# Performance work log

Measured on AMD Instinct MI355X. Metric: run time of the kernel, lower is better.

Reference implementation:

```python
import jax, jax.numpy as jnp
import numpy as np

B, C, H, W = 2, 64, 128, 128   # batch, z_dim, square feature map (original code requires H == W)
Q = 8192                       # query points per image
HID = 128                      # hidden_node
DIMS = [C * 9 + 4, HID, HID, HID, HID, C]
EPS_SHIFT = 1e-6
EPS_CLAMP = 1e-6


def setup_inputs():
    key = jax.random.key(0)
    ks = jax.random.split(key, 13)
    x = jax.random.normal(ks[0], (B, C, H, W), jnp.float32)
    coord = jax.random.uniform(ks[1], (B, Q, 2), jnp.float32, minval=-1.0, maxval=1.0)
    cell = jnp.full((B, Q, 2), 2.0 / 256.0, jnp.float32)  # cell of a 256x256 target grid
    inp = {"x": x, "coord": coord, "cell": cell}
    for i in range(5):
        fin, fout = DIMS[i], DIMS[i + 1]
        bound = 1.0 / np.sqrt(fin)
        inp[f"w{i}"] = jax.random.uniform(ks[3 + 2 * i], (fin, fout), jnp.float32, minval=-bound, maxval=bound)
        inp[f"b{i}"] = jax.random.uniform(ks[4 + 2 * i], (fout,), jnp.float32, minval=-bound, maxval=bound)
    return inp


def _unfold3x3(x):
    # F.unfold(x, 3, padding=1).view(B, C*9, H, W); channel order c*9 + (ky*3 + kx)
    b, c, h, w = x.shape
    xp = jnp.pad(x, ((0, 0), (0, 0), (1, 1), (1, 1)))
    pats = jnp.stack([xp[:, :, ky:ky + h, kx:kx + w] for ky in range(3) for kx in range(3)], axis=2)
    return pats.reshape(b, c * 9, h, w)


def _nearest_idx(g, n):
    # grid_sample mode='nearest', align_corners=False
    ix = ((g + 1.0) * n - 1.0) / 2.0
    return jnp.clip(jnp.round(ix), 0, n - 1).astype(jnp.int32)


def _liif_forward(x, coord, cell, w0, b0, w1, b1, w2, b2, w3, b3, w4, b4):
    b, c, h, w = x.shape
    feat = _unfold3x3(x)                                     # [B, 9C, H, W]
    feat_flat = feat.transpose(0, 2, 3, 1).reshape(b, h * w, 9 * c)
    # make_coord pixel-center sequence; H == W so one seq serves both axes
    seq = -1.0 + 1.0 / h + (2.0 / h) * jnp.arange(h, dtype=jnp.float32)
    rx = 1.0 / h   # 2 / H / 2
    ry = 1.0 / w
    hid_ws = [w0, w1, w2, w3]
    hid_bs = [b0, b1, b2, b3]
    scale = jnp.array([h, w], dtype=coord.dtype)
    rel_cell = cell * scale
    preds, areas = [], []
    for vx in (-1, 1):
        for vy in (-1, 1):
            c0 = jnp.clip(coord[..., 0] + vx * rx + EPS_SHIFT, -1 + EPS_CLAMP, 1 - EPS_CLAMP)
            c1 = jnp.clip(coord[..., 1] + vy * ry + EPS_SHIFT, -1 + EPS_CLAMP, 1 - EPS_CLAMP)
            # coord_.flip(-1): grid x (width) = coord[...,1], grid y (height) = coord[...,0]
            iy = _nearest_idx(c0, h)
            ix = _nearest_idx(c1, w)
            lin = iy * w + ix                                            # [B, Q]
            q_feat = jnp.take_along_axis(feat_flat, lin[..., None], axis=1)  # [B, Q, 9C]
            # feat_coord built with meshgrid(indexing='xy'): channel0 = seq[ix], channel1 = seq[iy]
            rel0 = (coord[..., 0] - seq[ix]) * h
            rel1 = (coord[..., 1] - seq[iy]) * w
            inp = jnp.concatenate([q_feat, rel0[..., None], rel1[..., None], rel_cell], axis=-1)
            hdd = inp
            for wi, bi in zip(hid_ws, hid_bs):
                hdd = jax.nn.relu(hdd @ wi + bi)
            preds.append(hdd @ w4 + b4)                                  # [B, Q, C]
            areas.append(jnp.abs(rel0 * rel1) + 1e-9)
    tot = areas[0] + areas[1] + areas[2] + areas[3]
    perm = (3, 2, 1, 0)   # original swaps areas 0<->3 and 1<->2
    ret = preds[0] * (areas[perm[0]] / tot)[..., None]
    for i in range(1, 4):
        ret = ret + preds[i] * (areas[perm[i]] / tot)[..., None]
    return ret


def reference(x, coord, cell, w0, b0, w1, b1, w2, b2, w3, b3, w4, b4):
    return _liif_forward(x, coord, cell, w0, b0, w1, b1, w2, b2, w3, b3, w4, b4)
```

## Files before the change

### kernel.cpp

```cpp
#include <hip/hip_runtime.h>


typedef unsigned short U16;
typedef unsigned int   u32;
using f16x8  = __attribute__((ext_vector_type(8)))  _Float16;
using f32x4  = __attribute__((ext_vector_type(4)))  float;
using f32x16 = __attribute__((ext_vector_type(16))) float;
using u16x8  = __attribute__((ext_vector_type(8)))  U16;
using u16x4  = __attribute__((ext_vector_type(4)))  U16;

#define P_OFF    2097152
#define W0F_OFF  6291456
#define W1F_OFF  6365184
#define W4F_OFF  6414336

__device__ __forceinline__ float h2f(U16 u){ _Float16 h; __builtin_memcpy(&h,&u,2); return (float)h; }
__device__ __forceinline__ U16 f2h(float f){ _Float16 h = (_Float16)f; U16 u; __builtin_memcpy(&u,&h,2); return u; }
__device__ __forceinline__ u32 packf16(float a, float b){
  _Float16 ha = (_Float16)a, hb = (_Float16)b;
  U16 ua, ub; __builtin_memcpy(&ua,&ha,2); __builtin_memcpy(&ub,&hb,2);
  return (u32)ua | ((u32)ub << 16);
}
__device__ __forceinline__ f16x8 bfrag(const u32* w){
  union { u32 u[4]; f16x8 v; } t;
  t.u[0]=w[0]; t.u[1]=w[1]; t.u[2]=w[2]; t.u[3]=w[3];
  return t.v;
}

__device__ __forceinline__ int nearest_idx(float g){
  float t = (g + 1.0f) * 128.0f;
  t = (t - 1.0f) * 0.5f;
  float r = rintf(t);
  r = fminf(fmaxf(r, 0.0f), 127.0f);
  return (int)r;
}
__device__ __forceinline__ float seqv(int i){ return -0.9921875f + 0.015625f*(float)i; }

__device__ __forceinline__ void corner_calc(float c0, float c1, int corner,
                                            int& iy, int& ix, float& rel0, float& rel1){
  const float rx = 0.0078125f;
  float sx = (corner & 2) ? rx : -rx;
  float sy = (corner & 1) ? rx : -rx;
  float a0 = c0 + sx; a0 = a0 + 1e-6f; a0 = fminf(fmaxf(a0, -1.0f + 1e-6f), 1.0f - 1e-6f);
  float a1 = c1 + sy; a1 = a1 + 1e-6f; a1 = fminf(fmaxf(a1, -1.0f + 1e-6f), 1.0f - 1e-6f);
  iy = nearest_idx(a0);
  ix = nearest_idx(a1);
  rel0 = (c0 - seqv(ix)) * 128.0f;
  rel1 = (c1 - seqv(iy)) * 128.0f;
}

__global__ __launch_bounds__(256) void k_prepw(
    const float* __restrict__ w0, const float* __restrict__ w1,
    const float* __restrict__ w2, const float* __restrict__ w3,
    const float* __restrict__ w4, U16* __restrict__ ws)
{
  __shared__ U16 sh[64 * 72];
  const int tid = threadIdx.x, bid = blockIdx.x;

  if (bid < 24) {
    int L = bid >> 3, s = bid & 7;
    const float* src = (L == 0) ? w1 : (L == 1) ? w2 : w3;
    {
      int kk = tid >> 4, m0 = (tid & 15) << 3;
      const float* p = src + (((s << 4) + kk) << 7) + m0;
      float4 a = *(const float4*)p, b2v = *(const float4*)(p + 4);
      U16* d = &sh[kk * 128 + m0];
      d[0]=f2h(a.x); d[1]=f2h(a.y); d[2]=f2h(a.z); d[3]=f2h(a.w);
      d[4]=f2h(b2v.x); d[5]=f2h(b2v.y); d[6]=f2h(b2v.z); d[7]=f2h(b2v.w);
    }
    __syncthreads();
    {
      int mt = tid >> 6, lane = tid & 63;
      u16x8 o;
      #pragma unroll
      for (int e = 0; e < 8; ++e)
        o[e] = sh[((((lane >> 5) << 3) + e) << 7) + (mt << 5) + (lane & 31)];
      *(u16x8*)(ws + W1F_OFF + (L << 14) + (((s << 2) + mt) << 9) + (lane << 3)) = o;
    }
  } else if (bid < 32) {
    int s = bid - 24;
    {
      int kk = tid >> 4, m0 = (tid & 15) << 2;
      float4 a = *(const float4*)(w4 + (((s << 4) + kk) << 6) + m0);
      U16* d = &sh[kk * 64 + m0];
      d[0]=f2h(a.x); d[1]=f2h(a.y); d[2]=f2h(a.z); d[3]=f2h(a.w);
    }
    __syncthreads();
    if (tid < 128) {
      int mt4 = tid >> 6, lane = tid & 63;
      u16x8 o;
      #pragma unroll
      for (int e = 0; e < 8; ++e)
        o[e] = sh[((((lane >> 5) << 3) + e) << 6) + (mt4 << 5) + (lane & 31)];
      *(u16x8*)(ws + W4F_OFF + (((s << 1) + mt4) << 9) + (lane << 3)) = o;
    }
  } else {
    int t2 = bid - 32, kpos = t2 >> 1, ks = t2 & 1;
    {
      int cc = tid >> 3, o0 = (tid & 7) << 4;
      const float* p = w0 + ((size_t)((((ks << 5) + cc) * 9) + kpos) << 7) + o0;
      #pragma unroll
      for (int j = 0; j < 4; ++j) {
        float4 v = *(const float4*)(p + (j << 2));
        U16* d = &sh[(cc << 7) + o0 + (j << 2)];
        d[0]=f2h(v.x); d[1]=f2h(v.y); d[2]=f2h(v.z); d[3]=f2h(v.w);
      }
    }
    __syncthreads();
    {
      int lane = tid & 63, mt0 = tid >> 6;
      #pragma unroll
      for (int i = 0; i < 2; ++i) {
        int mtile = mt0 + (i << 2);
        u16x8 o;
        #pragma unroll
        for (int e = 0; e < 8; ++e)
          o[e] = sh[((((lane >> 4) << 3) + e) << 7) + (mtile << 4) + (lane & 15)];
        *(u16x8*)(ws + W0F_OFF + (((((kpos << 1) + ks) << 3) + mtile) << 9) + (lane << 3)) = o;
      }
    }
  }
}

__global__ __launch_bounds__(256) void k_stage1(const float* __restrict__ x,
                                                const U16* __restrict__ w0f,
                                                const float* __restrict__ b0,
                                                U16* __restrict__ P)
{
  __shared__ U16 araw[3 * 66 * 64];
  const int tid = threadIdx.x, bid = blockIdx.x;
  const int b = bid >> 8, rem = bid & 255;
  const int y = rem >> 1, x0 = (rem & 1) << 6;

  {
    int c = tid & 63, dy = tid >> 6;
    if (dy < 3) {
      int yy = y + dy - 1;
      bool rowok = (yy >= 0) && (yy < 128);
      const float* xr = rowok
        ? (x + ((((size_t)b << 6) + c) << 14) + ((size_t)yy << 7)) : x;
      U16* arow = &araw[(dy * 66) * 64];
      {
        float v0 = 0.0f, v65 = 0.0f;
        if (rowok && x0 > 0)        v0  = xr[x0 - 1];
        if (rowok && x0 + 64 < 128) v65 = xr[x0 + 64];
        arow[0 * 64 + c] = f2h(v0);
        arow[65 * 64 + (c ^ 8)] = f2h(v65);
      }
      if (rowok) {
        #pragma unroll
        for (int g = 0; g < 16; ++g) {
          float4 v = *(const float4*)(xr + x0 + (g << 2));
          #pragma unroll
          for (int j = 0; j < 4; ++j) {
            int xp = 1 + (g << 2) + j;
            float vj = (j == 0) ? v.x : (j == 1) ? v.y : (j == 2) ? v.z : v.w;
            arow[xp * 64 + (c ^ ((xp & 7) << 3))] = f2h(vj);
          }
        }
      } else {
        #pragma unroll
        for (int xp = 1; xp <= 64; ++xp)
          arow[xp * 64 + (c ^ ((xp & 7) << 3))] = f2h(0.0f);
      }
    }
  }
  __syncthreads();

  const int wv = tid >> 6, ln = tid & 63;
  const int lrow = ln & 15, lg = ln >> 4;

  f32x4 acc[2][4];
  #pragma unroll
  for (int m = 0; m < 2; ++m)
    #pragma unroll
    for (int n = 0; n < 4; ++n) acc[m][n] = (f32x4){0.f, 0.f, 0.f, 0.f};

  #pragma unroll
  for (int kpos = 0; kpos < 9; ++kpos) {
    const int dyr = kpos / 3;
    const int dx = kpos % 3 - 1;
    f16x8 a[2][2];
    #pragma unroll
    for (int mf = 0; mf < 2; ++mf)
      #pragma unroll
      for (int ks = 0; ks < 2; ++ks) {
        size_t off = ((size_t)((((kpos << 1) + ks) << 3) + ((wv << 1) + mf)) << 9) + (ln << 3);
        a[mf][ks] = *(const f16x8*)(w0f + off);
      }
    #pragma unroll
    for (int ks = 0; ks < 2; ++ks)
      #pragma unroll
      for (int nf = 0; nf < 4; ++nf) {
        int xp = (nf << 4) + lrow + dx + 1;
        int cc = ((ks << 5) + (lg << 3)) ^ ((xp & 7) << 3);
        f16x8 bf = *(const f16x8*)(&araw[(dyr * 66 + xp) * 64 + cc]);
        acc[0][nf] = __builtin_amdgcn_mfma_f32_16x16x32_f16(a[0][ks], bf, acc[0][nf], 0, 0, 0);
        acc[1][nf] = __builtin_amdgcn_mfma_f32_16x16x32_f16(a[1][ks], bf, acc[1][nf], 0, 0, 0);
      }
  }

  #pragma unroll
  for (int mf = 0; mf < 2; ++mf) {
    int o0 = (wv << 5) + (mf << 4) + (lg << 2);
    float bb[4];
    #pragma unroll
    for (int r = 0; r < 4; ++r) bb[r] = b0[o0 + r];
    #pragma unroll
    for (int nf = 0; nf < 4; ++nf) {
      int px = x0 + (nf << 4) + lrow;
      u16x4 w;
      #pragma unroll
      for (int r = 0; r < 4; ++r) w[r] = f2h(acc[mf][nf][r] + bb[r]);
      *(u16x4*)(P + ((size_t)((b << 14) + (y << 7) + px)) * 128 + o0) = w;
    }
  }
}

__global__ __launch_bounds__(256) void k_stage2(
    const U16* __restrict__ P,
    const float* __restrict__ coord, const float* __restrict__ cell,
    const float* __restrict__ w0,
    const U16* __restrict__ w1f, const U16* __restrict__ w2f,
    const U16* __restrict__ w3f, const U16* __restrict__ w4f,
    const float* __restrict__ b1, const float* __restrict__ b2,
    const float* __restrict__ b3, const float* __restrict__ b4,
    float* __restrict__ out)
{
  const int tid = threadIdx.x;
  const int wv = tid >> 6, ln = tid & 63;
  const int wave = blockIdx.x * 4 + wv;
  const int q0 = wave << 3;
  const int col = ln & 31, h = ln >> 5;
  const int qi = col >> 2, c = col & 3;
  const int gq = q0 + qi;
  const int bimg = gq >> 13;

  float c0v = coord[gq * 2 + 0], c1v = coord[gq * 2 + 1];
  float rc0 = cell[gq * 2 + 0] * 128.0f, rc1 = cell[gq * 2 + 1] * 128.0f;
  int lin4[4]; float r0v[4], r1v[4], area[4];
  #pragma unroll
  for (int c4 = 0; c4 < 4; ++c4) {
    int iy, ix; float r0, r1;
    corner_calc(c0v, c1v, c4, iy, ix, r0, r1);
    lin4[c4] = iy * 128 + ix;
    r0v[c4] = r0; r1v[c4] = r1;
    area[c4] = fabsf(r0 * r1) + 1e-9f;
  }
  float tot = ((area[0] + area[1]) + area[2]) + area[3];
  float wgt = area[3 - c] / tot;
  float rel0 = r0v[c], rel1 = r1v[c];

  const U16* Pr = P + ((size_t)(bimg << 14) + lin4[c]) * 128;
  u16x8 pv[8];
  #pragma unroll
  for (int s = 0; s < 8; ++s)
    pv[s] = *(const u16x8*)(Pr + (s << 4) + (h << 3));

  u32 Bf[8][4];
  {
    const float* tu = w0 + 576 * 128;
    const float* tv = tu + 128;
    const float* ts2 = tv + 128;
    const float* tt = ts2 + 128;
    #pragma unroll
    for (int s = 0; s < 8; ++s) {
      int k0 = (s << 4) + (h << 3);
      f32x4 ua = *(const f32x4*)(tu + k0),  ub = *(const f32x4*)(tu + k0 + 4);
      f32x4 va = *(const f32x4*)(tv + k0),  vb = *(const f32x4*)(tv + k0 + 4);
      f32x4 sa = *(const f32x4*)(ts2 + k0), sb = *(const f32x4*)(ts2 + k0 + 4);
      f32x4 ta = *(const f32x4*)(tt + k0),  tb = *(const f32x4*)(tt + k0 + 4);
      float hh[8];
      #pragma unroll
      for (int e = 0; e < 8; ++e) {
        float uu = (e < 4) ? ua[e & 3] : ub[e & 3];
        float vvv = (e < 4) ? va[e & 3] : vb[e & 3];
        float ss = (e < 4) ? sa[e & 3] : sb[e & 3];
        float t2 = (e < 4) ? ta[e & 3] : tb[e & 3];
        hh[e] = fmaxf(h2f(pv[s][e]) + rel0 * uu + rel1 * vvv + rc0 * ss + rc1 * t2, 0.0f);
      }
      #pragma unroll
      for (int w = 0; w < 4; ++w)
        Bf[s][w] = packf16(hh[2 * w], hh[2 * w + 1]);
    }
  }

  const U16* wf_[3] = {w1f, w2f, w3f};
  const float* bL_[3] = {b1, b2, b3};
  #pragma unroll
  for (int L = 0; L < 3; ++L) {
    const U16* wf = wf_[L];
    const float* bL = bL_[L];
    f32x16 acc[4];
    #pragma unroll
    for (int mt = 0; mt < 4; ++mt)
      #pragma unroll
      for (int j = 0; j < 4; ++j) {
        f32x4 bv = *(const f32x4*)(bL + (mt << 5) + (j << 3) + (h << 2));
        #pragma unroll
        for (int q = 0; q < 4; ++q) acc[mt][4 * j + q] = bv[q];
      }
    #pragma unroll
    for (int s = 0; s < 8; ++s) {
      f16x8 B = bfrag(Bf[s]);
      #pragma unroll
      for (int mt = 0; mt < 4; ++mt) {
        f16x8 A = *(const f16x8*)(wf + (((size_t)(s * 4 + mt) * 64 + ln) << 3));
        acc[mt] = __builtin_amdgcn_mfma_f32_32x32x16_f16(A, B, acc[mt], 0, 0, 0);
      }
    }
    #pragma unroll
    for (int mtp = 0; mtp < 4; ++mtp) {
      u32 p[8];
      #pragma unroll
      for (int j2 = 0; j2 < 8; ++j2)
        p[j2] = packf16(fmaxf(acc[mtp][2 * j2], 0.0f), fmaxf(acc[mtp][2 * j2 + 1], 0.0f));
      #pragma unroll
      for (int u = 0; u < 2; ++u)
        #pragma unroll
        for (int w = 0; w < 2; ++w) {
          u32 va = p[w + 4 * u], vb = p[w + 4 * u + 2];
          asm("v_permlane32_swap_b32 %0, %1" : "+v"(va), "+v"(vb));
          Bf[2 * mtp + u][w]     = va;
          Bf[2 * mtp + u][w + 2] = vb;
        }
    }
  }

  f32x16 a4[2];
  #pragma unroll
  for (int mt4 = 0; mt4 < 2; ++mt4)
    #pragma unroll
    for (int r = 0; r < 16; ++r) a4[mt4][r] = 0.0f;
  #pragma unroll
  for (int s = 0; s < 8; ++s) {
    f16x8 B = bfrag(Bf[s]);
    #pragma unroll
    for (int mt4 = 0; mt4 < 2; ++mt4) {
      f16x8 A = *(const f16x8*)(w4f + (((size_t)(s * 2 + mt4) * 64 + ln) << 3));
      a4[mt4] = __builtin_amdgcn_mfma_f32_32x32x16_f16(A, B, a4[mt4], 0, 0, 0);
    }
  }

  float tacc[2][16];
  #pragma unroll
  for (int mt4 = 0; mt4 < 2; ++mt4)
    #pragma unroll
    for (int r = 0; r < 16; ++r) {
      float v = a4[mt4][r] * wgt;
      v += __shfl_xor(v, 1, 64);
      v += __shfl_xor(v, 2, 64);
      tacc[mt4][r] = v;
    }

  if (c == 0) {
    #pragma unroll
    for (int mt4 = 0; mt4 < 2; ++mt4)
      #pragma unroll
      for (int j = 0; j < 4; ++j) {
        int mo = (mt4 << 5) + (j << 3) + (h << 2);
        f32x4 bv = *(const f32x4*)(b4 + mo);
        f32x4 res;
        #pragma unroll
        for (int q = 0; q < 4; ++q) res[q] = tacc[mt4][4 * j + q] + bv[q];
        *(f32x4*)(out + (size_t)gq * 64 + mo) = res;
      }
  }
}

extern "C" void kernel_launch(void* const* d_in, const int* in_sizes, int n_in,
                              void* d_out, int out_size, void* d_ws, size_t ws_size,
                              hipStream_t stream)
{
  const float* x     = (const float*)d_in[0];
  const float* coord = (const float*)d_in[1];
  const float* cell  = (const float*)d_in[2];
  const float* w0    = (const float*)d_in[3];
  const float* b0    = (const float*)d_in[4];
  const float* w1    = (const float*)d_in[5];
  const float* b1    = (const float*)d_in[6];
  const float* w2    = (const float*)d_in[7];
  const float* b2    = (const float*)d_in[8];
  const float* w3    = (const float*)d_in[9];
  const float* b3    = (const float*)d_in[10];
  const float* w4    = (const float*)d_in[11];
  const float* b4    = (const float*)d_in[12];
  U16* ws = (U16*)d_ws;

  hipLaunchKernelGGL(k_prepw,  dim3(50),  dim3(256), 0, stream, w0, w1, w2, w3, w4, ws);
  hipLaunchKernelGGL(k_stage1, dim3(512), dim3(256), 0, stream,
                     x, ws + W0F_OFF, b0, ws + P_OFF);
  hipLaunchKernelGGL(k_stage2, dim3(512), dim3(256), 0, stream,
                     ws + P_OFF, coord, cell, w0,
                     ws + W1F_OFF, ws + W1F_OFF + 16384, ws + W1F_OFF + 32768, ws + W4F_OFF,
                     b1, b2, b3, b4, (float*)d_out);
}
```

Baseline: 44.44 us.

## Switch stage2 MLP to 16x16x32 MFMA with 4 queries per wave

Rewrites the per-query MLP in stage2 to use 16x16x32 f16 MFMA tiles instead of 32x32x16. Each wave now handles 4 queries (16 columns) rather than 8, and the grid doubles to 1024 blocks. The weight pre-swizzle in k_prepw is rewritten for the new fragment layout. The layer-to-layer fragment reshuffle now uses __shfl instead of permlane32 swaps. Smaller accumulators cut register pressure, and launch bounds request 4 blocks per SM to raise occupancy. The cost is more weight-fragment loads per query and extra cross-lane shuffle traffic.

```diff
diff --git a/kernel.cpp b/kernel.cpp
--- a/kernel.cpp
+++ b/kernel.cpp
@@ -5,14 +5,13 @@
 typedef unsigned int   u32;
 using f16x8  = __attribute__((ext_vector_type(8)))  _Float16;
 using f32x4  = __attribute__((ext_vector_type(4)))  float;
-using f32x16 = __attribute__((ext_vector_type(16))) float;
 using u16x8  = __attribute__((ext_vector_type(8)))  U16;
 using u16x4  = __attribute__((ext_vector_type(4)))  U16;
 
 #define P_OFF    2097152
 #define W0F_OFF  6291456
-#define W1F_OFF  6365184
-#define W4F_OFF  6414336
+#define W1G_OFF  6365184
+#define W4G_OFF  6414336
 
 __device__ __forceinline__ float h2f(U16 u){ _Float16 h; __builtin_memcpy(&h,&u,2); return (float)h; }
 __device__ __forceinline__ U16 f2h(float f){ _Float16 h = (_Float16)f; U16 u; __builtin_memcpy(&u,&h,2); return u; }
@@ -57,45 +56,53 @@
   __shared__ U16 sh[64 * 72];
   const int tid = threadIdx.x, bid = blockIdx.x;
 
-  if (bid < 24) {
-    int L = bid >> 3, s = bid & 7;
+  if (bid < 12) {
+    int L = bid >> 2, ks = bid & 3;
     const float* src = (L == 0) ? w1 : (L == 1) ? w2 : w3;
     {
-      int kk = tid >> 4, m0 = (tid & 15) << 3;
-      const float* p = src + (((s << 4) + kk) << 7) + m0;
-      float4 a = *(const float4*)p, b2v = *(const float4*)(p + 4);
-      U16* d = &sh[kk * 128 + m0];
+      int kl = tid >> 3, m0 = (tid & 7) << 4;
+      const float* p = src + (((ks << 5) + kl) << 7) + m0;
+      #pragma unroll
+      for (int j = 0; j < 4; ++j) {
+        float4 v = *(const float4*)(p + (j << 2));
+        U16* d = &sh[(kl << 7) + m0 + (j << 2)];
+        d[0]=f2h(v.x); d[1]=f2h(v.y); d[2]=f2h(v.z); d[3]=f2h(v.w);
+      }
+    }
+    __syncthreads();
+    {
+      int lane = tid & 63, mtb = tid >> 6;
+      #pragma unroll
+      for (int i = 0; i < 2; ++i) {
+        int mt = mtb + (i << 2);
+        u16x8 o;
+        #pragma unroll
+        for (int e = 0; e < 8; ++e)
+          o[e] = sh[((((lane >> 4) << 3) + e) << 7) + (mt << 4) + (lane & 15)];
+        *(u16x8*)(ws + W1G_OFF + (L << 14) + (((ks << 3) + mt) << 9) + (lane << 3)) = o;
+      }
+    }
+  } else if (bid < 16) {
+    int ks = bid - 12;
+    {
+      int kl = tid >> 3, m0 = (tid & 7) << 3;
+      const float* p = w4 + (((ks << 5) + kl) << 6) + m0;
+      float4 a = *(const float4*)p, b2 = *(const float4*)(p + 4);
+      U16* d = &sh[(kl << 6) + m0];
       d[0]=f2h(a.x); d[1]=f2h(a.y); d[2]=f2h(a.z); d[3]=f2h(a.w);
-      d[4]=f2h(b2v.x); d[5]=f2h(b2v.y); d[6]=f2h(b2v.z); d[7]=f2h(b2v.w);
+      d[4]=f2h(b2.x); d[5]=f2h(b2.y); d[6]=f2h(b2.z); d[7]=f2h(b2.w);
     }
     __syncthreads();
     {
-      int mt = tid >> 6, lane = tid & 63;
+      int lane = tid & 63, mt4 = tid >> 6;
       u16x8 o;
       #pragma unroll
       for (int e = 0; e < 8; ++e)
-        o[e] = sh[((((lane >> 5) << 3) + e) << 7) + (mt << 5) + (lane & 31)];
-      *(u16x8*)(ws + W1F_OFF + (L << 14) + (((s << 2) + mt) << 9) + (lane << 3)) = o;
-    }
-  } else if (bid < 32) {
-    int s = bid - 24;
-    {
-      int kk = tid >> 4, m0 = (tid & 15) << 2;
-      float4 a = *(const float4*)(w4 + (((s << 4) + kk) << 6) + m0);
-      U16* d = &sh[kk * 64 + m0];
-      d[0]=f2h(a.x); d[1]=f2h(a.y); d[2]=f2h(a.z); d[3]=f2h(a.w);
-    }
-    __syncthreads();
-    if (tid < 128) {
-      int mt4 = tid >> 6, lane = tid & 63;
-      u16x8 o;
-      #pragma unroll
-      for (int e = 0; e < 8; ++e)
-        o[e] = sh[((((lane >> 5) << 3) + e) << 6) + (mt4 << 5) + (lane & 31)];
-      *(u16x8*)(ws + W4F_OFF + (((s << 1) + mt4) << 9) + (lane << 3)) = o;
+        o[e] = sh[((((lane >> 4) << 3) + e) << 6) + (mt4 << 4) + (lane & 15)];
+      *(u16x8*)(ws + W4G_OFF + (((ks << 2) + mt4) << 9) + (lane << 3)) = o;
     }
   } else {
-    int t2 = bid - 32, kpos = t2 >> 1, ks = t2 & 1;
+    int t2 = bid - 16, kpos = t2 >> 1, ks = t2 & 1;
     {
       int cc = tid >> 3, o0 = (tid & 7) << 4;
       const float* p = w0 + ((size_t)((((ks << 5) + cc) * 9) + kpos) << 7) + o0;
@@ -217,12 +224,12 @@
   }
 }
 
-__global__ __launch_bounds__(256) void k_stage2(
+__global__ __launch_bounds__(256, 4) void k_stage2(
     const U16* __restrict__ P,
     const float* __restrict__ coord, const float* __restrict__ cell,
     const float* __restrict__ w0,
-    const U16* __restrict__ w1f, const U16* __restrict__ w2f,
-    const U16* __restrict__ w3f, const U16* __restrict__ w4f,
+    const U16* __restrict__ w1g, const U16* __restrict__ w2g,
+    const U16* __restrict__ w3g, const U16* __restrict__ w4g,
     const float* __restrict__ b1, const float* __restrict__ b2,
     const float* __restrict__ b3, const float* __restrict__ b4,
     float* __restrict__ out)
@@ -230,9 +237,9 @@
   const int tid = threadIdx.x;
   const int wv = tid >> 6, ln = tid & 63;
   const int wave = blockIdx.x * 4 + wv;
-  const int q0 = wave << 3;
-  const int col = ln & 31, h = ln >> 5;
-  const int qi = col >> 2, c = col & 3;
+  const int q0 = wave << 2;
+  const int c = ln & 15, h = ln >> 4;
+  const int qi = c >> 2, cc = c & 3;
   const int gq = q0 + qi;
   const int bimg = gq >> 13;
 
@@ -248,24 +255,20 @@
     area[c4] = fabsf(r0 * r1) + 1e-9f;
   }
   float tot = ((area[0] + area[1]) + area[2]) + area[3];
-  float wgt = area[3 - c] / tot;
-  float rel0 = r0v[c], rel1 = r1v[c];
-
-  const U16* Pr = P + ((size_t)(bimg << 14) + lin4[c]) * 128;
-  u16x8 pv[8];
-  #pragma unroll
-  for (int s = 0; s < 8; ++s)
-    pv[s] = *(const u16x8*)(Pr + (s << 4) + (h << 3));
-
-  u32 Bf[8][4];
+  float wgt = area[3 - cc] / tot;
+  float rel0 = r0v[cc], rel1 = r1v[cc];
+
+  u32 Bf[4][4];
   {
+    const U16* Pr = P + ((size_t)(bimg << 14) + lin4[cc]) * 128;
     const float* tu = w0 + 576 * 128;
     const float* tv = tu + 128;
     const float* ts2 = tv + 128;
     const float* tt = ts2 + 128;
     #pragma unroll
-    for (int s = 0; s < 8; ++s) {
-      int k0 = (s << 4) + (h << 3);
+    for (int ks = 0; ks < 4; ++ks) {
+      int k0 = (ks << 5) + (h << 3);
+      u16x8 pvv = *(const u16x8*)(Pr + k0);
       f32x4 ua = *(const f32x4*)(tu + k0),  ub = *(const f32x4*)(tu + k0 + 4);
       f32x4 va = *(const f32x4*)(tv + k0),  vb = *(const f32x4*)(tv + k0 + 4);
       f32x4 sa = *(const f32x4*)(ts2 + k0), sb = *(const f32x4*)(ts2 + k0 + 4);
@@ -273,98 +276,96 @@
       float hh[8];
       #pragma unroll
       for (int e = 0; e < 8; ++e) {
-        float uu = (e < 4) ? ua[e & 3] : ub[e & 3];
+        float uu  = (e < 4) ? ua[e & 3] : ub[e & 3];
         float vvv = (e < 4) ? va[e & 3] : vb[e & 3];
-        float ss = (e < 4) ? sa[e & 3] : sb[e & 3];
-        float t2 = (e < 4) ? ta[e & 3] : tb[e & 3];
-        hh[e] = fmaxf(h2f(pv[s][e]) + rel0 * uu + rel1 * vvv + rc0 * ss + rc1 * t2, 0.0f);
+        float ss  = (e < 4) ? sa[e & 3] : sb[e & 3];
+        float t2  = (e < 4) ? ta[e & 3] : tb[e & 3];
+        hh[e] = fmaxf(h2f(pvv[e]) + rel0 * uu + rel1 * vvv + rc0 * ss + rc1 * t2, 0.0f);
       }
       #pragma unroll
       for (int w = 0; w < 4; ++w)
-        Bf[s][w] = packf16(hh[2 * w], hh[2 * w + 1]);
-    }
-  }
-
-  const U16* wf_[3] = {w1f, w2f, w3f};
-  const float* bL_[3] = {b1, b2, b3};
+        Bf[ks][w] = packf16(hh[2 * w], hh[2 * w + 1]);
+    }
+  }
+
+  const int base = ((h & 1) << 5) | c;
+  const bool hi = (h & 2) != 0;
+
   #pragma unroll
   for (int L = 0; L < 3; ++L) {
-    const U16* wf = wf_[L];
-    const float* bL = bL_[L];
-    f32x16 acc[4];
-    #pragma unroll
-    for (int mt = 0; mt < 4; ++mt)
-      #pragma unroll
-      for (int j = 0; j < 4; ++j) {
-        f32x4 bv = *(const f32x4*)(bL + (mt << 5) + (j << 3) + (h << 2));
-        #pragma unroll
-        for (int q = 0; q < 4; ++q) acc[mt][4 * j + q] = bv[q];
-      }
-    #pragma unroll
-    for (int s = 0; s < 8; ++s) {
-      f16x8 B = bfrag(Bf[s]);
-      #pragma unroll
-      for (int mt = 0; mt < 4; ++mt) {
-        f16x8 A = *(const f16x8*)(wf + (((size_t)(s * 4 + mt) * 64 + ln) << 3));
-        acc[mt] = __builtin_amdgcn_mfma_f32_32x32x16_f16(A, B, acc[mt], 0, 0, 0);
-      }
-    }
-    #pragma unroll
-    for (int mtp = 0; mtp < 4; ++mtp) {
-      u32 p[8];
-      #pragma unroll
-      for (int j2 = 0; j2 < 8; ++j2)
-        p[j2] = packf16(fmaxf(acc[mtp][2 * j2], 0.0f), fmaxf(acc[mtp][2 * j2 + 1], 0.0f));
-      #pragma unroll
-      for (int u = 0; u < 2; ++u)
-        #pragma unroll
-        for (int w = 0; w < 2; ++w) {
-          u32 va = p[w + 4 * u], vb = p[w + 4 * u + 2];
-          asm("v_permlane32_swap_b32 %0, %1" : "+v"(va), "+v"(vb));
-          Bf[2 * mtp + u][w]     = va;
-          Bf[2 * mtp + u][w + 2] = vb;
-        }
-    }
-  }
-
-  f32x16 a4[2];
-  #pragma unroll
-  for (int mt4 = 0; mt4 < 2; ++mt4)
-    #pragma unroll
-    for (int r = 0; r < 16; ++r) a4[mt4][r] = 0.0f;
-  #pragma unroll
-  for (int s = 0; s < 8; ++s) {
-    f16x8 B = bfrag(Bf[s]);
-    #pragma unroll
-    for (int mt4 = 0; mt4 < 2; ++mt4) {
-      f16x8 A = *(const f16x8*)(w4f + (((size_t)(s * 2 + mt4) * 64 + ln) << 3));
-      a4[mt4] = __builtin_amdgcn_mfma_f32_32x32x16_f16(A, B, a4[mt4], 0, 0, 0);
-    }
-  }
-
-  float tacc[2][16];
-  #pragma unroll
-  for (int mt4 = 0; mt4 < 2; ++mt4)
-    #pragma unroll
-    for (int r = 0; r < 16; ++r) {
+    const U16* wg = (L == 0) ? w1g : (L == 1) ? w2g : w3g;
+    const float* bL = (L == 0) ? b1 : (L == 1) ? b2 : b3;
+    f32x4 acc[8];
+    #pragma unroll
+    for (int mt = 0; mt < 8; ++mt)
+      acc[mt] = *(const f32x4*)(bL + (mt << 4) + (h << 2));
+    #pragma unroll
+    for (int ks = 0; ks < 4; ++ks) {
+      f16x8 B = bfrag(Bf[ks]);
+      #pragma unroll
+      for (int mt = 0; mt < 8; ++mt) {
+        f16x8 A = *(const f16x8*)(wg + (((ks << 3) + mt) << 9) + (ln << 3));
+        acc[mt] = __builtin_amdgcn_mfma_f32_16x16x32_f16(A, B, acc[mt], 0, 0, 0);
+      }
+    }
+    u32 pk[8][2];
+    #pragma unroll
+    for (int mt = 0; mt < 8; ++mt)
+      #pragma unroll
+      for (int p = 0; p < 2; ++p)
+        pk[mt][p] = packf16(fmaxf(acc[mt][2 * p], 0.0f),
+                            fmaxf(acc[mt][2 * p + 1], 0.0f));
+    #pragma unroll
+    for (int ks = 0; ks < 4; ++ks) {
+      u32 a0 = __shfl(pk[2 * ks][0],     base,      64);
+      u32 a1 = __shfl(pk[2 * ks][1],     base,      64);
+      u32 a2 = __shfl(pk[2 * ks][0],     base + 16, 64);
+      u32 a3 = __shfl(pk[2 * ks][1],     base + 16, 64);
+      u32 b0v = __shfl(pk[2 * ks + 1][0], base,      64);
+      u32 b1v = __shfl(pk[2 * ks + 1][1], base,      64);
+      u32 b2v = __shfl(pk[2 * ks + 1][0], base + 16, 64);
+      u32 b3v = __shfl(pk[2 * ks + 1][1], base + 16, 64);
+      Bf[ks][0] = hi ? b0v : a0;
+      Bf[ks][1] = hi ? b1v : a1;
+      Bf[ks][2] = hi ? b2v : a2;
+      Bf[ks][3] = hi ? b3v : a3;
+    }
+  }
+
+  f32x4 a4[4];
+  #pragma unroll
+  for (int mt4 = 0; mt4 < 4; ++mt4) a4[mt4] = (f32x4){0.f, 0.f, 0.f, 0.f};
+  #pragma unroll
+  for (int ks = 0; ks < 4; ++ks) {
+    f16x8 B = bfrag(Bf[ks]);
+    #pragma unroll
+    for (int mt4 = 0; mt4 < 4; ++mt4) {
+      f16x8 A = *(const f16x8*)(w4g + (((ks << 2) + mt4) << 9) + (ln << 3));
+      a4[mt4] = __builtin_amdgcn_mfma_f32_16x16x32_f16(A, B, a4[mt4], 0, 0, 0);
+    }
+  }
+
+  float tacc[4][4];
+  #pragma unroll
+  for (int mt4 = 0; mt4 < 4; ++mt4)
+    #pragma unroll
+    for (int r = 0; r < 4; ++r) {
       float v = a4[mt4][r] * wgt;
       v += __shfl_xor(v, 1, 64);
       v += __shfl_xor(v, 2, 64);
       tacc[mt4][r] = v;
     }
 
-  if (c == 0) {
-    #pragma unroll
-    for (int mt4 = 0; mt4 < 2; ++mt4)
-      #pragma unroll
-      for (int j = 0; j < 4; ++j) {
-        int mo = (mt4 << 5) + (j << 3) + (h << 2);
-        f32x4 bv = *(const f32x4*)(b4 + mo);
-        f32x4 res;
-        #pragma unroll
-        for (int q = 0; q < 4; ++q) res[q] = tacc[mt4][4 * j + q] + bv[q];
-        *(f32x4*)(out + (size_t)gq * 64 + mo) = res;
-      }
+  if (cc == 0) {
+    #pragma unroll
+    for (int mt4 = 0; mt4 < 4; ++mt4) {
+      int mo = (mt4 << 4) + (h << 2);
+      f32x4 bv = *(const f32x4*)(b4 + mo);
+      f32x4 res;
+      #pragma unroll
+      for (int r = 0; r < 4; ++r) res[r] = tacc[mt4][r] + bv[r];
+      *(f32x4*)(out + (size_t)gq * 64 + mo) = res;
+    }
   }
 }
 
@@ -387,11 +388,11 @@
   const float* b4    = (const float*)d_in[12];
   U16* ws = (U16*)d_ws;
 
-  hipLaunchKernelGGL(k_prepw,  dim3(50),  dim3(256), 0, stream, w0, w1, w2, w3, w4, ws);
-  hipLaunchKernelGGL(k_stage1, dim3(512), dim3(256), 0, stream,
+  hipLaunchKernelGGL(k_prepw,  dim3(34),   dim3(256), 0, stream, w0, w1, w2, w3, w4, ws);
+  hipLaunchKernelGGL(k_stage1, dim3(512),  dim3(256), 0, stream,
                      x, ws + W0F_OFF, b0, ws + P_OFF);
-  hipLaunchKernelGGL(k_stage2, dim3(512), dim3(256), 0, stream,
+  hipLaunchKernelGGL(k_stage2, dim3(1024), dim3(256), 0, stream,
                      ws + P_OFF, coord, cell, w0,
-                     ws + W1F_OFF, ws + W1F_OFF + 16384, ws + W1F_OFF + 32768, ws + W4F_OFF,
+                     ws + W1G_OFF, ws + W1G_OFF + 16384, ws + W1G_OFF + 32768, ws + W4G_OFF,
                      b1, b2, b3, b4, (float*)d_out);
 }
```

New measurement: 58.05 us. 1.31x slower.

## Software-pipeline weight fragment loads across MLP layers in stage2

Applied to the files above, without the earlier changes.

Weight A-fragments for the hidden and final layers are now loaded into a register ring of four stages ahead of use. Loads for the next layer are issued while the MFMAs of the current layer run, and sched_barrier fences pin the order. The aim is to hide global/L2 load latency behind matrix work. It adds __syncthreads after each layer, which were not needed before since waves are independent, and it raises register pressure.

```diff
diff --git a/kernel.cpp b/kernel.cpp
--- a/kernel.cpp
+++ b/kernel.cpp
@@ -216,6 +216,31 @@
     }
   }
 }
+
+#define LDA4(dst, base, sidx) \
+  dst[0] = *(const f16x8*)((base) + ((((sidx) << 2) + 0) << 9) + lnoff); \
+  dst[1] = *(const f16x8*)((base) + ((((sidx) << 2) + 1) << 9) + lnoff); \
+  dst[2] = *(const f16x8*)((base) + ((((sidx) << 2) + 2) << 9) + lnoff); \
+  dst[3] = *(const f16x8*)((base) + ((((sidx) << 2) + 3) << 9) + lnoff);
+#define LDA2(dst, base, sidx) \
+  dst[0] = *(const f16x8*)((base) + ((((sidx) << 1) + 0) << 9) + lnoff); \
+  dst[1] = *(const f16x8*)((base) + ((((sidx) << 1) + 1) << 9) + lnoff);
+#define HSTEP(s, AB, RF) do { \
+  f16x8 Bv = bfrag(Bf[s]); \
+  acc[0] = __builtin_amdgcn_mfma_f32_32x32x16_f16(AB[0], Bv, acc[0], 0, 0, 0); \
+  acc[1] = __builtin_amdgcn_mfma_f32_32x32x16_f16(AB[1], Bv, acc[1], 0, 0, 0); \
+  acc[2] = __builtin_amdgcn_mfma_f32_32x32x16_f16(AB[2], Bv, acc[2], 0, 0, 0); \
+  acc[3] = __builtin_amdgcn_mfma_f32_32x32x16_f16(AB[3], Bv, acc[3], 0, 0, 0); \
+  RF \
+  __builtin_amdgcn_sched_barrier(0); \
+} while (0)
+#define FSTEP(s, AB, RF) do { \
+  f16x8 Bv = bfrag(Bf[s]); \
+  a4[0] = __builtin_amdgcn_mfma_f32_32x32x16_f16(AB[0], Bv, a4[0], 0, 0, 0); \
+  a4[1] = __builtin_amdgcn_mfma_f32_32x32x16_f16(AB[1], Bv, a4[1], 0, 0, 0); \
+  RF \
+  __builtin_amdgcn_sched_barrier(0); \
+} while (0)
 
 __global__ __launch_bounds__(256) void k_stage2(
     const U16* __restrict__ P,
@@ -235,6 +260,7 @@
   const int qi = col >> 2, c = col & 3;
   const int gq = q0 + qi;
   const int bimg = gq >> 13;
+  const int lnoff = ln << 3;
 
   float c0v = coord[gq * 2 + 0], c1v = coord[gq * 2 + 1];
   float rc0 = cell[gq * 2 + 0] * 128.0f, rc1 = cell[gq * 2 + 1] * 128.0f;
@@ -256,6 +282,10 @@
   #pragma unroll
   for (int s = 0; s < 8; ++s)
     pv[s] = *(const u16x8*)(Pr + (s << 4) + (h << 3));
+
+  f16x8 A0[4], A1[4], A2[4], A3[4];
+  LDA4(A0, w1f, 0) LDA4(A1, w1f, 1) LDA4(A2, w1f, 2) LDA4(A3, w1f, 3)
+  __builtin_amdgcn_sched_barrier(0);
 
   u32 Bf[8][4];
   {
@@ -273,10 +303,10 @@
       float hh[8];
       #pragma unroll
       for (int e = 0; e < 8; ++e) {
-        float uu = (e < 4) ? ua[e & 3] : ub[e & 3];
+        float uu  = (e < 4) ? ua[e & 3] : ub[e & 3];
         float vvv = (e < 4) ? va[e & 3] : vb[e & 3];
-        float ss = (e < 4) ? sa[e & 3] : sb[e & 3];
-        float t2 = (e < 4) ? ta[e & 3] : tb[e & 3];
+        float ss  = (e < 4) ? sa[e & 3] : sb[e & 3];
+        float t2  = (e < 4) ? ta[e & 3] : tb[e & 3];
         hh[e] = fmaxf(h2f(pv[s][e]) + rel0 * uu + rel1 * vvv + rc0 * ss + rc1 * t2, 0.0f);
       }
       #pragma unroll
@@ -284,12 +314,15 @@
         Bf[s][w] = packf16(hh[2 * w], hh[2 * w + 1]);
     }
   }
+  __syncthreads();
 
   const U16* wf_[3] = {w1f, w2f, w3f};
+  const U16* wn_[3] = {w2f, w3f, w4f};
   const float* bL_[3] = {b1, b2, b3};
   #pragma unroll
   for (int L = 0; L < 3; ++L) {
     const U16* wf = wf_[L];
+    const U16* wn = wn_[L];
     const float* bL = bL_[L];
     f32x16 acc[4];
     #pragma unroll
@@ -300,14 +333,20 @@
         #pragma unroll
         for (int q = 0; q < 4; ++q) acc[mt][4 * j + q] = bv[q];
       }
-    #pragma unroll
-    for (int s = 0; s < 8; ++s) {
-      f16x8 B = bfrag(Bf[s]);
-      #pragma unroll
-      for (int mt = 0; mt < 4; ++mt) {
-        f16x8 A = *(const f16x8*)(wf + (((size_t)(s * 4 + mt) * 64 + ln) << 3));
-        acc[mt] = __builtin_amdgcn_mfma_f32_32x32x16_f16(A, B, acc[mt], 0, 0, 0);
-      }
+    HSTEP(0, A0, LDA4(A0, wf, 4));
+    HSTEP(1, A1, LDA4(A1, wf, 5));
+    HSTEP(2, A2, LDA4(A2, wf, 6));
+    HSTEP(3, A3, LDA4(A3, wf, 7));
+    if (L < 2) {
+      HSTEP(4, A0, LDA4(A0, wn, 0));
+      HSTEP(5, A1, LDA4(A1, wn, 1));
+      HSTEP(6, A2, LDA4(A2, wn, 2));
+      HSTEP(7, A3, LDA4(A3, wn, 3));
+    } else {
+      HSTEP(4, A0, LDA2(A0, w4f, 0));
+      HSTEP(5, A1, LDA2(A1, w4f, 1));
+      HSTEP(6, A2, LDA2(A2, w4f, 2));
+      HSTEP(7, A3, LDA2(A3, w4f, 3));
     }
     #pragma unroll
     for (int mtp = 0; mtp < 4; ++mtp) {
@@ -325,6 +364,7 @@
           Bf[2 * mtp + u][w + 2] = vb;
         }
     }
+    __syncthreads();
   }
 
   f32x16 a4[2];
@@ -332,15 +372,14 @@
   for (int mt4 = 0; mt4 < 2; ++mt4)
     #pragma unroll
     for (int r = 0; r < 16; ++r) a4[mt4][r] = 0.0f;
-  #pragma unroll
-  for (int s = 0; s < 8; ++s) {
-    f16x8 B = bfrag(Bf[s]);
-    #pragma unroll
-    for (int mt4 = 0; mt4 < 2; ++mt4) {
-      f16x8 A = *(const f16x8*)(w4f + (((size_t)(s * 2 + mt4) * 64 + ln) << 3));
-      a4[mt4] = __builtin_amdgcn_mfma_f32_32x32x16_f16(A, B, a4[mt4], 0, 0, 0);
-    }
-  }
+  FSTEP(0, A0, LDA2(A0, w4f, 4));
+  FSTEP(1, A1, LDA2(A1, w4f, 5));
+  FSTEP(2, A2, LDA2(A2, w4f, 6));
+  FSTEP(3, A3, LDA2(A3, w4f, 7));
+  FSTEP(4, A0, );
+  FSTEP(5, A1, );
+  FSTEP(6, A2, );
+  FSTEP(7, A3, );
 
   float tacc[2][16];
   #pragma unroll
```

Result: slower. 46.79 us (+5.3%).
